# Kernel optimization log

Measured on AMD Instinct MI355X. Metric: run time of the kernel, lower is better.

## Reference

```python
import jax, jax.numpy as jnp
import numpy as np

B, T, C, H = 16, 2048, 1024, 64

def setup_inputs() -> dict:
    key = jax.random.key(0)
    kx, kq, kk, kv = jax.random.split(key, 4)
    s = 0.02
    return {
        "x": jax.random.normal(kx, (B, T, C), dtype=jnp.float32),
        "Wq": jax.random.normal(kq, (C, H), dtype=jnp.float32) * s,
        "Wk": jax.random.normal(kk, (C, H), dtype=jnp.float32) * s,
        "Wv": jax.random.normal(kv, (C, H), dtype=jnp.float32) * s,
    }

def reference(x, Wq, Wk, Wv):
    Bc, Tc, Cc = x.shape
    q = x @ Wq  # [B,T,H]
    k = x @ Wk  # [B,T,H]
    v = x @ Wv  # [B,T,H]
    # NOTE: original scales by n_embed^{-0.5} (C), not head_size^{-0.5}
    wei = jnp.einsum("bth,bsh->bts", q, k) * (Cc ** -0.5)  # [B,T,T]
    causal = jnp.tril(jnp.ones((Tc, Tc), dtype=bool))
    wei = jnp.where(causal, wei, -jnp.inf)
    wei = jax.nn.softmax(wei, axis=-1)
    # dropout is identity in eval mode
    out = jnp.einsum("bts,bsh->bth", wei, v)  # [B,T,H]
    return out
```

## Files before the change

### kernel.cpp

```cpp
#include <hip/hip_runtime.h>

typedef __attribute__((ext_vector_type(8))) short short8;
typedef __attribute__((ext_vector_type(4))) float float4v;

__device__ inline short f2bf(float f) {
    union { float f; unsigned int u; } c; c.f = f;
    unsigned int u = c.u;
    unsigned int r = (u + 0x7fffu + ((u >> 16) & 1u)) >> 16;
    return (short)r;
}

__device__ inline short8 pack8_cvt(float4 a, float4 b) {
    union { short8 s; unsigned int u[4]; } r;
    asm("v_cvt_pk_bf16_f32 %0, %1, %2" : "=v"(r.u[0]) : "v"(a.x), "v"(a.y));
    asm("v_cvt_pk_bf16_f32 %0, %1, %2" : "=v"(r.u[1]) : "v"(a.z), "v"(a.w));
    asm("v_cvt_pk_bf16_f32 %0, %1, %2" : "=v"(r.u[2]) : "v"(b.x), "v"(b.y));
    asm("v_cvt_pk_bf16_f32 %0, %1, %2" : "=v"(r.u[3]) : "v"(b.z), "v"(b.w));
    return r.s;
}

__device__ inline void gl2lds16(const short* g, short* l) {
    __builtin_amdgcn_global_load_lds(
        (const __attribute__((address_space(1))) unsigned int*)g,
        (__attribute__((address_space(3))) unsigned int*)l, 16, 0, 0);
}


__global__ __launch_bounds__(256) void wconv_kernel(
    const float* __restrict__ Wq, const float* __restrict__ Wk,
    const float* __restrict__ Wv, short* __restrict__ Wt_s)
{
    __shared__ short Ls[64 * 72];
    const int w  = blockIdx.x >> 4;
    const int c  = blockIdx.x & 15;
    const int k0 = c * 64;
    const float* W = (w == 0) ? Wq : (w == 1) ? Wk : Wv;
    const int tid = threadIdx.x;

#pragma unroll
    for (int i = 0; i < 4; i++) {
        int kk = (tid >> 4) + i * 16;
        int c4 = (tid & 15) * 4;
        float4 v = *(const float4*)&W[(size_t)(k0 + kk) * 64 + c4];
        Ls[kk * 72 + c4 + 0] = f2bf(v.x);
        Ls[kk * 72 + c4 + 1] = f2bf(v.y);
        Ls[kk * 72 + c4 + 2] = f2bf(v.z);
        Ls[kk * 72 + c4 + 3] = f2bf(v.w);
    }
    __syncthreads();
    const int n  = tid >> 2;
    const int k8 = (tid & 3) * 16;
    short8 o0, o1;
#pragma unroll
    for (int j = 0; j < 8; j++) o0[j] = Ls[(k8 + j) * 72 + n];
#pragma unroll
    for (int j = 0; j < 8; j++) o1[j] = Ls[(k8 + 8 + j) * 72 + n];
    const int gn = w * 64 + n;
    short* base = &Wt_s[((size_t)c * 192 + gn) * 64];
    int g0 = k8 >> 3;
    *(short8*)&base[((g0    ) ^ (gn & 7)) * 8] = o0;
    *(short8*)&base[((g0 + 1) ^ (gn & 7)) * 8] = o1;
}

__global__ __launch_bounds__(256) void qkv_kernel(
    const float* __restrict__ x, const short* __restrict__ Wt_s,
    short* __restrict__ qo, short* __restrict__ k_s, short* __restrict__ vT_t)
{
    __shared__ short As[2][64 * 72];
    __shared__ short Bs[2][192 * 64];

    const int tid  = threadIdx.x;
    const int wave = tid >> 6, lane = tid & 63;
    const int quad = lane >> 4, l16 = lane & 15;
    const int m0   = blockIdx.x * 64;

    float4v acc[4][3];
#pragma unroll
    for (int mf = 0; mf < 4; mf++)
#pragma unroll
        for (int nt = 0; nt < 3; nt++) acc[mf][nt] = (float4v)0.0f;

    const int arow = tid >> 2;
    const int acol = (tid & 3) * 16;
    const float* ap = &x[(size_t)(m0 + arow) * 1024 + acol];
    const int lofs = lane * 8;

    {
        float4 x0 = *(const float4*)(ap);
        float4 x1 = *(const float4*)(ap + 4);
        float4 x2 = *(const float4*)(ap + 8);
        float4 x3 = *(const float4*)(ap + 12);
        const short* gsrc = Wt_s + ((size_t)wave * 48) * 64;
        short* ldst = &Bs[0][wave * 48 * 64];
#pragma unroll
        for (int i = 0; i < 6; i++)
            gl2lds16(gsrc + i * 512 + lofs, ldst + i * 512 + lofs);
        *(short8*)&As[0][arow * 72 + acol]     = pack8_cvt(x0, x1);
        *(short8*)&As[0][arow * 72 + acol + 8] = pack8_cvt(x2, x3);
    }
    __syncthreads();

    int cur = 0;
    for (int kc = 0; kc < 1024; kc += 64) {
        const int nxt = cur ^ 1;
        const bool pf = (kc + 64) < 1024;
        float4 x0, x1, x2, x3;
        if (pf) {
            x0 = *(const float4*)(ap + kc + 64);
            x1 = *(const float4*)(ap + kc + 68);
            x2 = *(const float4*)(ap + kc + 72);
            x3 = *(const float4*)(ap + kc + 76);
            const short* gsrc = Wt_s + ((size_t)((kc >> 6) + 1) * 192 + wave * 48) * 64;
            short* ldst = &Bs[nxt][wave * 48 * 64];
#pragma unroll
            for (int i = 0; i < 6; i++)
                gl2lds16(gsrc + i * 512 + lofs, ldst + i * 512 + lofs);
        }
        const short* Asc = As[cur];
        const short* Bsc = Bs[cur];
#pragma unroll
        for (int kc2 = 0; kc2 < 2; kc2++) {
            short8 a0 = *(const short8*)&Asc[(     l16) * 72 + kc2*32 + quad*8];
            short8 a1 = *(const short8*)&Asc[(16 + l16) * 72 + kc2*32 + quad*8];
            short8 a2 = *(const short8*)&Asc[(32 + l16) * 72 + kc2*32 + quad*8];
            short8 a3 = *(const short8*)&Asc[(48 + l16) * 72 + kc2*32 + quad*8];
#pragma unroll
            for (int nt = 0; nt < 3; nt++) {
                int brow = wave * 48 + nt * 16 + l16;
                int g = kc2 * 4 + quad;
                short8 bf = *(const short8*)&Bsc[brow * 64 + (g ^ (brow & 7)) * 8];
                acc[0][nt] = __builtin_amdgcn_mfma_f32_16x16x32_bf16(a0, bf, acc[0][nt], 0, 0, 0);
                acc[1][nt] = __builtin_amdgcn_mfma_f32_16x16x32_bf16(a1, bf, acc[1][nt], 0, 0, 0);
                acc[2][nt] = __builtin_amdgcn_mfma_f32_16x16x32_bf16(a2, bf, acc[2][nt], 0, 0, 0);
                acc[3][nt] = __builtin_amdgcn_mfma_f32_16x16x32_bf16(a3, bf, acc[3][nt], 0, 0, 0);
            }
        }
        if (pf) {
            *(short8*)&As[nxt][arow * 72 + acol]     = pack8_cvt(x0, x1);
            *(short8*)&As[nxt][arow * 72 + acol + 8] = pack8_cvt(x2, x3);
        }
        __syncthreads();
        cur = nxt;
    }
#pragma unroll
    for (int mf = 0; mf < 4; mf++) {
#pragma unroll
        for (int nt = 0; nt < 3; nt++) {
            int g = wave * 48 + nt * 16 + l16;
#pragma unroll
            for (int r = 0; r < 4; r++) {
                int row = m0 + mf * 16 + quad * 4 + r;
                short val = f2bf(acc[mf][nt][r]);
                if (g < 64) {
                    qo[(size_t)row * 64 + g] = val;
                } else if (g < 128) {
                    int h = g - 64;
                    k_s[(size_t)row * 64 + (((h >> 3) ^ (row & 7)) * 8 + (h & 7))] = val;
                } else {
                    int h = g - 128;
                    int bb = row >> 11, tt = row & 2047;
                    int tc = tt >> 6, tl = tt & 63;
                    vT_t[(((size_t)bb * 32 + tc) * 64 + h) * 64 +
                         (((tl >> 3) ^ (h & 7)) * 8 + (tl & 7))] = val;
                }
            }
        }
    }
}

#define SCALE_LOG2E 0.04508422132f

__global__ __launch_bounds__(256) void attn_kernel(
    const short* __restrict__ q, const short* __restrict__ k_s,
    const short* __restrict__ vT_t, float* __restrict__ out)
{
    __shared__ short Ks[2][64 * 64];
    __shared__ short Vs[2][64 * 64];
    __shared__ short Ps[64 * 72];

    const int tid  = threadIdx.x;
    const int wave = tid >> 6, lane = tid & 63;
    const int quad = lane >> 4, l16 = lane & 15;

    int b, qt;
    if (blockIdx.x < 256) { b = blockIdx.x >> 4; qt = 16 + (blockIdx.x & 15); }
    else { int t2 = blockIdx.x - 256; b = t2 >> 4; qt = 15 - (t2 & 15); }

    const short* kb = k_s  + (size_t)b * 2048 * 64;
    const short* vb = vT_t + (size_t)b * 32 * 64 * 64;

    const short* qrow = q + ((size_t)b * 2048 + qt*64 + wave*16 + l16) * 64;
    short8 qf0 = *(const short8*)&qrow[quad*8];
    short8 qf1 = *(const short8*)&qrow[32 + quad*8];

    float4v oacc[4];
#pragma unroll
    for (int t = 0; t < 4; t++) oacc[t] = (float4v)0.0f;
    float l_i[4] = {0.f, 0.f, 0.f, 0.f};

    const int tg   = qt*64 + wave*16 + quad*4;
    const int jmax = qt;
    const int lofs = lane * 8;

    {
        const short* kg = kb + ((size_t)wave * 16) * 64;
        short* kl = &Ks[0][wave * 16 * 64];
        gl2lds16(kg +       lofs, kl +       lofs);
        gl2lds16(kg + 512 + lofs, kl + 512 + lofs);
        const short* vg = vb + ((size_t)wave * 16) * 64;
        short* vl = &Vs[0][wave * 16 * 64];
        gl2lds16(vg +       lofs, vl +       lofs);
        gl2lds16(vg + 512 + lofs, vl + 512 + lofs);
    }
    __syncthreads();

    int cur = 0;
    for (int j = 0; j <= jmax; j++) {
        const int nxt = cur ^ 1;
        if (j < jmax) {
            const short* kg = kb + ((size_t)(j + 1) * 64 + wave * 16) * 64;
            short* kl = &Ks[nxt][wave * 16 * 64];
            gl2lds16(kg +       lofs, kl +       lofs);
            gl2lds16(kg + 512 + lofs, kl + 512 + lofs);
            const short* vg = vb + ((size_t)(j + 1) * 64 + wave * 16) * 64;
            short* vl = &Vs[nxt][wave * 16 * 64];
            gl2lds16(vg +       lofs, vl +       lofs);
            gl2lds16(vg + 512 + lofs, vl + 512 + lofs);
        }
        const short* Ksc = Ks[cur];
        const short* Vsc = Vs[cur];

        float4v sacc[4];
#pragma unroll
        for (int t = 0; t < 4; t++) sacc[t] = (float4v)0.0f;
#pragma unroll
        for (int t = 0; t < 4; t++) {
            int brow = t*16 + l16;
            short8 b0 = *(const short8*)&Ksc[brow * 64 + ((    quad) ^ (brow & 7)) * 8];
            short8 b1 = *(const short8*)&Ksc[brow * 64 + ((4 + quad) ^ (brow & 7)) * 8];
            sacc[t] = __builtin_amdgcn_mfma_f32_16x16x32_bf16(qf0, b0, sacc[t], 0, 0, 0);
            sacc[t] = __builtin_amdgcn_mfma_f32_16x16x32_bf16(qf1, b1, sacc[t], 0, 0, 0);
        }
        if (j == jmax) {
#pragma unroll
            for (int t = 0; t < 4; t++) {
                int sg = j*64 + t*16 + l16;
#pragma unroll
                for (int r = 0; r < 4; r++) {
                    float p = exp2f(sacc[t][r] * SCALE_LOG2E);
                    if (sg > tg + r) p = 0.0f;
                    sacc[t][r] = p;
                    l_i[r] += p;
                }
            }
        } else {
#pragma unroll
            for (int t = 0; t < 4; t++)
#pragma unroll
                for (int r = 0; r < 4; r++) {
                    float p = exp2f(sacc[t][r] * SCALE_LOG2E);
                    sacc[t][r] = p;
                    l_i[r] += p;
                }
        }
#pragma unroll
        for (int t = 0; t < 4; t++)
#pragma unroll
            for (int r = 0; r < 4; r++)
                Ps[(wave*16 + quad*4 + r) * 72 + t*16 + l16] = f2bf(sacc[t][r]);
#pragma unroll
        for (int kc = 0; kc < 2; kc++) {
            short8 af = *(const short8*)&Ps[(wave*16 + l16) * 72 + kc*32 + quad*8];
#pragma unroll
            for (int t = 0; t < 4; t++) {
                int drow = t*16 + l16;
                short8 bf = *(const short8*)&Vsc[drow * 64 + ((kc*4 + quad) ^ (drow & 7)) * 8];
                oacc[t] = __builtin_amdgcn_mfma_f32_16x16x32_bf16(af, bf, oacc[t], 0, 0, 0);
            }
        }
        __syncthreads();
        cur = nxt;
    }
#pragma unroll
    for (int off = 1; off < 16; off <<= 1)
#pragma unroll
        for (int r = 0; r < 4; r++)
            l_i[r] += __shfl_xor(l_i[r], off, 64);
#pragma unroll
    for (int r = 0; r < 4; r++) {
        float inv = 1.0f / l_i[r];
        int row = qt*64 + wave*16 + quad*4 + r;
#pragma unroll
        for (int t = 0; t < 4; t++)
            out[((size_t)b * 2048 + row) * 64 + t*16 + l16] = oacc[t][r] * inv;
    }
}

extern "C" void kernel_launch(void* const* d_in, const int* in_sizes, int n_in,
                              void* d_out, int out_size, void* d_ws, size_t ws_size,
                              hipStream_t stream)
{
    const float* x  = (const float*)d_in[0];
    const float* Wq = (const float*)d_in[1];
    const float* Wk = (const float*)d_in[2];
    const float* Wv = (const float*)d_in[3];

    short* qw   = (short*)d_ws;
    short* ks   = qw + (size_t)32768 * 64;
    short* vTt  = ks + (size_t)32768 * 64;
    short* Wts  = vTt + (size_t)32768 * 64;
    float* out  = (float*)d_out;

    hipLaunchKernelGGL(wconv_kernel, dim3(48), dim3(256), 0, stream,
                       Wq, Wk, Wv, Wts);
    hipLaunchKernelGGL(qkv_kernel, dim3(512), dim3(256), 0, stream,
                       x, Wts, qw, ks, vTt);
    hipLaunchKernelGGL(attn_kernel, dim3(512), dim3(256), 0, stream,
                       qw, ks, vTt, out);
}
```

Measured before the change: 251.3 us.

## Use a four-slot K/V ring and compute two tiles per barrier

Grows the shared K/V buffers from two slots to four. Each loop iteration now prefetches the next two 64-key tiles while it computes the current two, so there is one __syncthreads per two tiles instead of one per tile, plus a tail step for odd tile counts. The aim is to halve barrier stalls and keep loads further ahead of compute. In exchange, LDS use roughly doubles for K/V, which may lower the number of blocks that fit on each CU.

```diff
diff --git a/kernel.cpp b/kernel.cpp
--- a/kernel.cpp
+++ b/kernel.cpp
@@ -170,12 +170,76 @@
 
 #define SCALE_LOG2E 0.04508422132f
 
+#define STAGE_KV(SLOT, JT) do {                                          \
+    const short* kg = kb + ((size_t)(JT) * 64 + wave * 16) * 64;         \
+    short* kl = &Ks[SLOT][wave * 16 * 64];                               \
+    gl2lds16(kg +       lofs, kl +       lofs);                          \
+    gl2lds16(kg + 512 + lofs, kl + 512 + lofs);                          \
+    const short* vg = vb + ((size_t)(JT) * 64 + wave * 16) * 64;         \
+    short* vl = &Vs[SLOT][wave * 16 * 64];                               \
+    gl2lds16(vg +       lofs, vl +       lofs);                          \
+    gl2lds16(vg + 512 + lofs, vl + 512 + lofs);                          \
+} while (0)
+
+#define COMPUTE_TILE(SLOT, JC) do {                                      \
+    const short* Ksc = Ks[SLOT];                                         \
+    const short* Vsc = Vs[SLOT];                                         \
+    float4v sacc[4];                                                     \
+    _Pragma("unroll")                                                    \
+    for (int t = 0; t < 4; t++) sacc[t] = (float4v)0.0f;                 \
+    _Pragma("unroll")                                                    \
+    for (int t = 0; t < 4; t++) {                                        \
+        int brow = t*16 + l16;                                           \
+        short8 b0 = *(const short8*)&Ksc[brow * 64 + ((    quad) ^ (brow & 7)) * 8]; \
+        short8 b1 = *(const short8*)&Ksc[brow * 64 + ((4 + quad) ^ (brow & 7)) * 8]; \
+        sacc[t] = __builtin_amdgcn_mfma_f32_16x16x32_bf16(qf0, b0, sacc[t], 0, 0, 0); \
+        sacc[t] = __builtin_amdgcn_mfma_f32_16x16x32_bf16(qf1, b1, sacc[t], 0, 0, 0); \
+    }                                                                    \
+    if ((JC) == jmax) {                                                  \
+        _Pragma("unroll")                                                \
+        for (int t = 0; t < 4; t++) {                                    \
+            int sg = (JC)*64 + t*16 + l16;                               \
+            _Pragma("unroll")                                            \
+            for (int r = 0; r < 4; r++) {                                \
+                float p = exp2f(sacc[t][r] * SCALE_LOG2E);               \
+                if (sg > tg + r) p = 0.0f;                               \
+                sacc[t][r] = p;                                          \
+                l_i[r] += p;                                             \
+            }                                                            \
+        }                                                                \
+    } else {                                                             \
+        _Pragma("unroll")                                                \
+        for (int t = 0; t < 4; t++)                                      \
+            _Pragma("unroll")                                            \
+            for (int r = 0; r < 4; r++) {                                \
+                float p = exp2f(sacc[t][r] * SCALE_LOG2E);               \
+                sacc[t][r] = p;                                          \
+                l_i[r] += p;                                             \
+            }                                                            \
+    }                                                                    \
+    _Pragma("unroll")                                                    \
+    for (int t = 0; t < 4; t++)                                          \
+        _Pragma("unroll")                                                \
+        for (int r = 0; r < 4; r++)                                      \
+            Ps[(wave*16 + quad*4 + r) * 72 + t*16 + l16] = f2bf(sacc[t][r]); \
+    _Pragma("unroll")                                                    \
+    for (int kc = 0; kc < 2; kc++) {                                     \
+        short8 af = *(const short8*)&Ps[(wave*16 + l16) * 72 + kc*32 + quad*8]; \
+        _Pragma("unroll")                                                \
+        for (int t = 0; t < 4; t++) {                                    \
+            int drow = t*16 + l16;                                       \
+            short8 bf = *(const short8*)&Vsc[drow * 64 + ((kc*4 + quad) ^ (drow & 7)) * 8]; \
+            oacc[t] = __builtin_amdgcn_mfma_f32_16x16x32_bf16(af, bf, oacc[t], 0, 0, 0); \
+        }                                                                \
+    }                                                                    \
+} while (0)
+
 __global__ __launch_bounds__(256) void attn_kernel(
     const short* __restrict__ q, const short* __restrict__ k_s,
     const short* __restrict__ vT_t, float* __restrict__ out)
 {
-    __shared__ short Ks[2][64 * 64];
-    __shared__ short Vs[2][64 * 64];
+    __shared__ short Ks[4][64 * 64];
+    __shared__ short Vs[4][64 * 64];
     __shared__ short Ps[64 * 72];
 
     const int tid  = threadIdx.x;
@@ -202,85 +266,22 @@
     const int jmax = qt;
     const int lofs = lane * 8;
 
-    {
-        const short* kg = kb + ((size_t)wave * 16) * 64;
-        short* kl = &Ks[0][wave * 16 * 64];
-        gl2lds16(kg +       lofs, kl +       lofs);
-        gl2lds16(kg + 512 + lofs, kl + 512 + lofs);
-        const short* vg = vb + ((size_t)wave * 16) * 64;
-        short* vl = &Vs[0][wave * 16 * 64];
-        gl2lds16(vg +       lofs, vl +       lofs);
-        gl2lds16(vg + 512 + lofs, vl + 512 + lofs);
-    }
+    STAGE_KV(0, 0);
+    if (jmax >= 1) STAGE_KV(1, 1);
     __syncthreads();
 
-    int cur = 0;
-    for (int j = 0; j <= jmax; j++) {
-        const int nxt = cur ^ 1;
-        if (j < jmax) {
-            const short* kg = kb + ((size_t)(j + 1) * 64 + wave * 16) * 64;
-            short* kl = &Ks[nxt][wave * 16 * 64];
-            gl2lds16(kg +       lofs, kl +       lofs);
-            gl2lds16(kg + 512 + lofs, kl + 512 + lofs);
-            const short* vg = vb + ((size_t)(j + 1) * 64 + wave * 16) * 64;
-            short* vl = &Vs[nxt][wave * 16 * 64];
-            gl2lds16(vg +       lofs, vl +       lofs);
-            gl2lds16(vg + 512 + lofs, vl + 512 + lofs);
-        }
-        const short* Ksc = Ks[cur];
-        const short* Vsc = Vs[cur];
-
-        float4v sacc[4];
-#pragma unroll
-        for (int t = 0; t < 4; t++) sacc[t] = (float4v)0.0f;
-#pragma unroll
-        for (int t = 0; t < 4; t++) {
-            int brow = t*16 + l16;
-            short8 b0 = *(const short8*)&Ksc[brow * 64 + ((    quad) ^ (brow & 7)) * 8];
-            short8 b1 = *(const short8*)&Ksc[brow * 64 + ((4 + quad) ^ (brow & 7)) * 8];
-            sacc[t] = __builtin_amdgcn_mfma_f32_16x16x32_bf16(qf0, b0, sacc[t], 0, 0, 0);
-            sacc[t] = __builtin_amdgcn_mfma_f32_16x16x32_bf16(qf1, b1, sacc[t], 0, 0, 0);
-        }
-        if (j == jmax) {
-#pragma unroll
-            for (int t = 0; t < 4; t++) {
-                int sg = j*64 + t*16 + l16;
-#pragma unroll
-                for (int r = 0; r < 4; r++) {
-                    float p = exp2f(sacc[t][r] * SCALE_LOG2E);
-                    if (sg > tg + r) p = 0.0f;
-                    sacc[t][r] = p;
-                    l_i[r] += p;
-                }
-            }
-        } else {
-#pragma unroll
-            for (int t = 0; t < 4; t++)
-#pragma unroll
-                for (int r = 0; r < 4; r++) {
-                    float p = exp2f(sacc[t][r] * SCALE_LOG2E);
-                    sacc[t][r] = p;
-                    l_i[r] += p;
-                }
-        }
-#pragma unroll
-        for (int t = 0; t < 4; t++)
-#pragma unroll
-            for (int r = 0; r < 4; r++)
-                Ps[(wave*16 + quad*4 + r) * 72 + t*16 + l16] = f2bf(sacc[t][r]);
-#pragma unroll
-        for (int kc = 0; kc < 2; kc++) {
-            short8 af = *(const short8*)&Ps[(wave*16 + l16) * 72 + kc*32 + quad*8];
-#pragma unroll
-            for (int t = 0; t < 4; t++) {
-                int drow = t*16 + l16;
-                short8 bf = *(const short8*)&Vsc[drow * 64 + ((kc*4 + quad) ^ (drow & 7)) * 8];
-                oacc[t] = __builtin_amdgcn_mfma_f32_16x16x32_bf16(af, bf, oacc[t], 0, 0, 0);
-            }
-        }
+    int j = 0;
+    for (; j + 1 <= jmax; j += 2) {
+        if (j + 2 <= jmax) STAGE_KV((j + 2) & 3, j + 2);
+        if (j + 3 <= jmax) STAGE_KV((j + 3) & 3, j + 3);
+        COMPUTE_TILE(j & 3, j);
+        COMPUTE_TILE((j + 1) & 3, j + 1);
         __syncthreads();
-        cur = nxt;
-    }
+    }
+    if (j == jmax) {
+        COMPUTE_TILE(j & 3, j);
+    }
+
 #pragma unroll
     for (int off = 1; off < 16; off <<= 1)
 #pragma unroll
```

New measurement: 243.3 us. 1.03x faster.
